# Kernel optimization log

Measured on AMD Instinct MI355X. Metric: run time of the kernel, lower is better.

Reference implementation:

```python
import jax, jax.numpy as jnp
import numpy as np

B, T, D_IN, D_OUT, N_HEAD = 2, 2048, 1024, 1024, 16
HEAD_DIM = D_OUT // N_HEAD


def setup_inputs() -> dict:
    key = jax.random.key(0)
    k1, k2, k3, k4 = jax.random.split(key, 4)
    s = 0.02  # init scale for weights
    return {
        "x": jax.random.normal(k1, (B, T, D_IN), jnp.float32),
        "Wq": jax.random.normal(k2, (D_OUT, D_IN), jnp.float32) * s,
        "Wk": jax.random.normal(k3, (D_OUT, D_IN), jnp.float32) * s,
        "Wv": jax.random.normal(k4, (D_OUT, D_IN), jnp.float32) * s,
    }


def reference(x, Wq, Wk, Wv):
    b, t, _ = x.shape
    h, hd = N_HEAD, HEAD_DIM
    # Linear projections (torch Linear: x @ W.T), split heads -> [b,h,t,hd]
    q = (x @ Wq.T).reshape(b, t, h, hd).transpose(0, 2, 1, 3)
    k = (x @ Wk.T).reshape(b, t, h, hd).transpose(0, 2, 1, 3)
    v = (x @ Wv.T).reshape(b, t, h, hd).transpose(0, 2, 1, 3)
    # raw scores [b,h,t,t], causal mask BEFORE scaling (as in source)
    omega = jnp.einsum("bhqd,bhkd->bhqk", q, k)
    causal = jnp.triu(jnp.ones((t, t), dtype=bool), k=1)
    omega = jnp.where(causal, -jnp.inf, omega)
    attw = jax.nn.softmax(omega / jnp.sqrt(jnp.asarray(hd, omega.dtype)), axis=-1)
    ctx = jnp.einsum("bhqk,bhkd->bhqd", attw, v)  # [b,h,t,hd]
    # Faithful to source: transpose(2,3) then view(B,T,d_out)
    out = jnp.swapaxes(ctx, 2, 3).reshape(b, t, D_OUT)
    return out
```

## Files before the change

kernel.cpp:

```cpp
#include <hip/hip_runtime.h>
#include <hip/hip_bf16.h>
#include <stdint.h>

typedef __attribute__((ext_vector_type(8))) short s16x8;
typedef __attribute__((ext_vector_type(4))) float f32x4;

#define T_   2048
#define NH   16
#define HD   64
#define DIN  1024
#define SCALE_LOG2 0.18033688011112042f

#define MFMA32(a, b, c) __builtin_amdgcn_mfma_f32_16x16x32_bf16(a, b, c, 0, 0, 0)

__device__ __forceinline__ unsigned short f2bf(float f) {
  union { float f; uint32_t u; } c; c.f = f;
  uint32_t u = c.u;
  return (unsigned short)((u + 0x7FFFu + ((u >> 16) & 1u)) >> 16);
}

__device__ __forceinline__ uint32_t pk_bf16(float a, float b) {
  __hip_bfloat162 h = __float22bfloat162_rn(make_float2(a, b));
  return *reinterpret_cast<uint32_t*>(&h);
}

#define GLL(gp, lp) __builtin_amdgcn_global_load_lds( \
    (__attribute__((address_space(1))) void*)(gp),    \
    (__attribute__((address_space(3))) void*)(lp), 16, 0, 0)

__global__ __launch_bounds__(256) void cvt_kernel(
    const float* __restrict__ x,  const float* __restrict__ wq,
    const float* __restrict__ wk, const float* __restrict__ wv,
    unsigned short* __restrict__ xb, unsigned short* __restrict__ wb) {
  int i = (blockIdx.x * 256 + threadIdx.x) * 4;
  float4 v;
  unsigned short* dp;
  if (i < 4194304) {
    v = *(const float4*)(x + i);
    dp = xb + i;
  } else {
    int j = i - 4194304;
    int seg = j >> 20, r = j & 1048575;
    const float* w = (seg == 0) ? wq : (seg == 1) ? wk : wv;
    v = *(const float4*)(w + r);
    dp = wb + j;
  }
  ushort4 o;
  o.x = f2bf(v.x); o.y = f2bf(v.y); o.z = f2bf(v.z); o.w = f2bf(v.w);
  *(ushort4*)dp = o;
}

__global__ __launch_bounds__(256) void qkv_gemm(
    const unsigned short* __restrict__ A, const unsigned short* __restrict__ Bm,
    unsigned short* __restrict__ qkv) {
  __shared__ __attribute__((aligned(16))) unsigned short Alds[64 * 64];
  __shared__ __attribute__((aligned(16))) unsigned short Blds[128 * 64];
  const int tid = threadIdx.x;
  const int lane = tid & 63, wave = tid >> 6;
  const int wm = wave >> 1, wn = wave & 1;
  const int m0 = blockIdx.y * 64, n0 = blockIdx.x * 128;

  f32x4 acc[2][4] = {};

  const int srA = wave * 16 + (lane >> 3);
  const int srB = wave * 32 + (lane >> 3);
  const int scol = (((lane & 7) ^ ((lane >> 3) & 7))) * 8;
  const unsigned short* ag = A  + (size_t)(m0 + srA) * DIN + scol;
  const unsigned short* bg = Bm + (size_t)(n0 + srB) * DIN + scol;
  unsigned short* al = &Alds[wave * 16 * 64];
  unsigned short* bl = &Blds[wave * 32 * 64];

  const int l16 = lane & 15, quad = lane >> 4;
  const int sw = l16 & 7;

  for (int k0 = 0; k0 < DIN; k0 += 64) {
    __syncthreads();
#pragma unroll
    for (int i = 0; i < 2; i++)
      GLL(ag + (size_t)i * 8 * DIN + k0, al + i * 512);
#pragma unroll
    for (int i = 0; i < 4; i++)
      GLL(bg + (size_t)i * 8 * DIN + k0, bl + i * 512);
    __syncthreads();
#pragma unroll
    for (int ks = 0; ks < 2; ks++) {
      const int cl = ((ks * 4 + quad) ^ sw) * 8;
      s16x8 af[2], bf[4];
#pragma unroll
      for (int mt = 0; mt < 2; mt++)
        af[mt] = *(const s16x8*)&Alds[(wm * 32 + mt * 16 + l16) * 64 + cl];
#pragma unroll
      for (int nt = 0; nt < 4; nt++)
        bf[nt] = *(const s16x8*)&Blds[(wn * 64 + nt * 16 + l16) * 64 + cl];
#pragma unroll
      for (int mt = 0; mt < 2; mt++)
#pragma unroll
        for (int nt = 0; nt < 4; nt++)
          acc[mt][nt] = MFMA32(af[mt], bf[nt], acc[mt][nt]);
    }
  }

#pragma unroll
  for (int mt = 0; mt < 2; mt++) {
    int mbase = m0 + wm * 32 + mt * 16 + (quad << 2);
    int b = mbase >> 11, t = mbase & 2047;
#pragma unroll
    for (int nt = 0; nt < 4; nt++) {
      int n = n0 + wn * 64 + nt * 16 + l16;
      int sel = n >> 10, h = (n >> 6) & 15, d = n & 63;
      int bh = b * NH + h;
      if (sel == 2) {
        ushort4 pk;
        pk.x = f2bf(acc[mt][nt][0]); pk.y = f2bf(acc[mt][nt][1]);
        pk.z = f2bf(acc[mt][nt][2]); pk.w = f2bf(acc[mt][nt][3]);
        *(ushort4*)&qkv[8388608 + (size_t)(bh * HD + d) * T_ + t] = pk;
      } else {
        float qs = (sel == 0) ? SCALE_LOG2 : 1.f;
#pragma unroll
        for (int r = 0; r < 4; r++)
          qkv[(size_t)sel * 4194304 + (size_t)(bh * T_ + t + r) * HD + d] =
              f2bf(acc[mt][nt][r] * qs);
      }
    }
  }
}

__global__ __launch_bounds__(256) void attn_kernel(
    const unsigned short* __restrict__ qkv, float* __restrict__ out) {
  __shared__ __attribute__((aligned(16))) unsigned short Klds[64 * 64];
  __shared__ __attribute__((aligned(16))) unsigned short Vt[64 * 64];
  __shared__ __attribute__((aligned(16))) unsigned short Plds[64 * 64];

  const int lane = threadIdx.x & 63, wave = threadIdx.x >> 6;
  const int l16 = lane & 15, quad = lane >> 4;
  const int swl = l16 & 7;
  const int qt = 31 - blockIdx.y, bh = blockIdx.x;
  const int q0 = qt * 64;
  const size_t bh_off = (size_t)bh * (T_ * HD);
  const unsigned short* Q  = qkv + bh_off;
  const unsigned short* Kb = qkv + 4194304 + bh_off;
  const unsigned short* Vb = qkv + 8388608 + bh_off;

  s16x8 qf[2];
  {
    const unsigned short* qp =
        Q + (size_t)(q0 + wave * 16 + l16) * HD + quad * 8;
    qf[0] = *(const s16x8*)(qp);
    qf[1] = *(const s16x8*)(qp + 32);
  }

  const int sr = threadIdx.x >> 3;
  const int sc = (threadIdx.x & 7) * 8;
  const int swc = (((threadIdx.x & 7) ^ (sr & 7))) * 8;

  s16x8 kr0 = *(const s16x8*)&Kb[(size_t)sr * HD + sc];
  s16x8 kr1 = *(const s16x8*)&Kb[(size_t)(sr + 32) * HD + sc];
  s16x8 vr0 = *(const s16x8*)&Vb[(size_t)sr * T_ + sc];
  s16x8 vr1 = *(const s16x8*)&Vb[(size_t)(sr + 32) * T_ + sc];

  const s16x8 onesf = {0x3F80, 0x3F80, 0x3F80, 0x3F80,
                       0x3F80, 0x3F80, 0x3F80, 0x3F80};
  f32x4 o[4] = {};
  f32x4 lacc = {};

  uint32_t* prow = (uint32_t*)&Plds[(wave * 16 + l16) * 64];
  const unsigned short* prd = &Plds[(wave * 16 + l16) * 64];

  for (int kt = 0; kt <= qt; kt++) {
    __syncthreads();
    *(s16x8*)&Klds[sr * 64 + swc] = kr0;
    *(s16x8*)&Klds[(sr + 32) * 64 + swc] = kr1;
    *(s16x8*)&Vt[sr * 64 + swc] = vr0;
    *(s16x8*)&Vt[(sr + 32) * 64 + swc] = vr1;
    if (kt < qt) {
      const unsigned short* kp = Kb + (size_t)(kt + 1) * 64 * HD;
      const unsigned short* vp = Vb + (kt + 1) * 64;
      kr0 = *(const s16x8*)&kp[(size_t)sr * HD + sc];
      kr1 = *(const s16x8*)&kp[(size_t)(sr + 32) * HD + sc];
      vr0 = *(const s16x8*)&vp[(size_t)sr * T_ + sc];
      vr1 = *(const s16x8*)&vp[(size_t)(sr + 32) * T_ + sc];
    }
    __syncthreads();

    f32x4 s[4] = {};
#pragma unroll
    for (int kk = 0; kk < 2; kk++) {
      const int cl = ((kk * 4 + quad) ^ swl) * 8;
#pragma unroll
      for (int nt = 0; nt < 4; nt++) {
        s16x8 kf = *(const s16x8*)&Klds[(nt * 16 + l16) * 64 + cl];
        s[nt] = MFMA32(kf, qf[kk], s[nt]);
      }
    }

    if (kt < qt) {
#pragma unroll
      for (int nt = 0; nt < 4; nt++) {
        float p0 = exp2f(s[nt][0]);
        float p1 = exp2f(s[nt][1]);
        float p2 = exp2f(s[nt][2]);
        float p3 = exp2f(s[nt][3]);
        *(uint2*)&prow[(((2 * nt + (quad >> 1)) ^ swl) << 2) + (quad & 1) * 2] =
            make_uint2(pk_bf16(p0, p1), pk_bf16(p2, p3));
      }
    } else {
      const int lim = wave * 16 + l16;
#pragma unroll
      for (int nt = 0; nt < 4; nt++) {
        const int kb = nt * 16 + quad * 4;
        float p0 = (kb + 0 <= lim) ? exp2f(s[nt][0]) : 0.f;
        float p1 = (kb + 1 <= lim) ? exp2f(s[nt][1]) : 0.f;
        float p2 = (kb + 2 <= lim) ? exp2f(s[nt][2]) : 0.f;
        float p3 = (kb + 3 <= lim) ? exp2f(s[nt][3]) : 0.f;
        *(uint2*)&prow[(((2 * nt + (quad >> 1)) ^ swl) << 2) + (quad & 1) * 2] =
            make_uint2(pk_bf16(p0, p1), pk_bf16(p2, p3));
      }
    }

#pragma unroll
    for (int kk = 0; kk < 2; kk++) {
      const int cl = ((kk * 4 + quad) ^ swl) * 8;
      s16x8 pf = *(const s16x8*)&prd[cl];
      lacc = MFMA32(pf, onesf, lacc);
#pragma unroll
      for (int dt = 0; dt < 4; dt++) {
        s16x8 vf = *(const s16x8*)&Vt[(dt * 16 + l16) * 64 + cl];
        o[dt] = MFMA32(pf, vf, o[dt]);
      }
    }
  }

  f32x4 inv;
#pragma unroll
  for (int r = 0; r < 4; r++) inv[r] = 1.f / lacc[r];
#pragma unroll
  for (int dt = 0; dt < 4; dt++) {
    float4 v = make_float4(o[dt][0] * inv[0], o[dt][1] * inv[1],
                           o[dt][2] * inv[2], o[dt][3] * inv[3]);
    *(float4*)(out + (size_t)bh * (HD * T_) + (size_t)(dt * 16 + l16) * T_ +
               q0 + wave * 16 + quad * 4) = v;
  }
}

extern "C" void kernel_launch(void* const* d_in, const int* in_sizes, int n_in,
                              void* d_out, int out_size, void* d_ws, size_t ws_size,
                              hipStream_t stream) {
  const float* x  = (const float*)d_in[0];
  const float* wq = (const float*)d_in[1];
  const float* wk = (const float*)d_in[2];
  const float* wv = (const float*)d_in[3];
  float* out = (float*)d_out;

  unsigned short* xb  = (unsigned short*)d_ws;
  unsigned short* wb  = xb + 4194304;
  unsigned short* qkv = wb + 3145728;

  cvt_kernel<<<7168, 256, 0, stream>>>(x, wq, wk, wv, xb, wb);
  dim3 g1(24, 64);
  qkv_gemm<<<g1, 256, 0, stream>>>(xb, wb, qkv);
  dim3 g2(32, 32);
  attn_kernel<<<g2, 256, 0, stream>>>(qkv, out);
}
```

Before: 150.5 us.

## Keep softmax probabilities in registers and feed PV via 16x16x16 MFMA

```diff
diff --git a/kernel.cpp b/kernel.cpp
--- a/kernel.cpp
+++ b/kernel.cpp
@@ -3,6 +3,7 @@
 #include <stdint.h>
 
 typedef __attribute__((ext_vector_type(8))) short s16x8;
+typedef __attribute__((ext_vector_type(4))) short s16x4;
 typedef __attribute__((ext_vector_type(4))) float f32x4;
 
 #define T_   2048
@@ -12,6 +13,16 @@
 #define SCALE_LOG2 0.18033688011112042f
 
 #define MFMA32(a, b, c) __builtin_amdgcn_mfma_f32_16x16x32_bf16(a, b, c, 0, 0, 0)
+
+__device__ __forceinline__ f32x4 mfma16(s16x4 a, s16x4 b, f32x4 c) {
+#if __has_builtin(__builtin_amdgcn_mfma_f32_16x16x16bf16_1k)
+  return __builtin_amdgcn_mfma_f32_16x16x16bf16_1k(a, b, c, 0, 0, 0);
+#else
+  s16x8 a8 = {a[0], a[1], a[2], a[3], 0, 0, 0, 0};
+  s16x8 b8 = {b[0], b[1], b[2], b[3], 0, 0, 0, 0};
+  return __builtin_amdgcn_mfma_f32_16x16x32_bf16(a8, b8, c, 0, 0, 0);
+#endif
+}
 
 __device__ __forceinline__ unsigned short f2bf(float f) {
   union { float f; uint32_t u; } c; c.f = f;
@@ -129,7 +140,6 @@
     const unsigned short* __restrict__ qkv, float* __restrict__ out) {
   __shared__ __attribute__((aligned(16))) unsigned short Klds[64 * 64];
   __shared__ __attribute__((aligned(16))) unsigned short Vt[64 * 64];
-  __shared__ __attribute__((aligned(16))) unsigned short Plds[64 * 64];
 
   const int lane = threadIdx.x & 63, wave = threadIdx.x >> 6;
   const int l16 = lane & 15, quad = lane >> 4;
@@ -158,13 +168,9 @@
   s16x8 vr0 = *(const s16x8*)&Vb[(size_t)sr * T_ + sc];
   s16x8 vr1 = *(const s16x8*)&Vb[(size_t)(sr + 32) * T_ + sc];
 
-  const s16x8 onesf = {0x3F80, 0x3F80, 0x3F80, 0x3F80,
-                       0x3F80, 0x3F80, 0x3F80, 0x3F80};
+  const s16x4 ones4 = {0x3F80, 0x3F80, 0x3F80, 0x3F80};
   f32x4 o[4] = {};
   f32x4 lacc = {};
-
-  uint32_t* prow = (uint32_t*)&Plds[(wave * 16 + l16) * 64];
-  const unsigned short* prd = &Plds[(wave * 16 + l16) * 64];
 
   for (int kt = 0; kt <= qt; kt++) {
     __syncthreads();
@@ -193,6 +199,7 @@
       }
     }
 
+    s16x4 pf[4];
     if (kt < qt) {
 #pragma unroll
       for (int nt = 0; nt < 4; nt++) {
@@ -200,8 +207,9 @@
         float p1 = exp2f(s[nt][1]);
         float p2 = exp2f(s[nt][2]);
         float p3 = exp2f(s[nt][3]);
-        *(uint2*)&prow[(((2 * nt + (quad >> 1)) ^ swl) << 2) + (quad & 1) * 2] =
-            make_uint2(pk_bf16(p0, p1), pk_bf16(p2, p3));
+        union { s16x4 v; uint2 u; } pu;
+        pu.u = make_uint2(pk_bf16(p0, p1), pk_bf16(p2, p3));
+        pf[nt] = pu.v;
       }
     } else {
       const int lim = wave * 16 + l16;
@@ -212,20 +220,23 @@
         float p1 = (kb + 1 <= lim) ? exp2f(s[nt][1]) : 0.f;
         float p2 = (kb + 2 <= lim) ? exp2f(s[nt][2]) : 0.f;
         float p3 = (kb + 3 <= lim) ? exp2f(s[nt][3]) : 0.f;
-        *(uint2*)&prow[(((2 * nt + (quad >> 1)) ^ swl) << 2) + (quad & 1) * 2] =
-            make_uint2(pk_bf16(p0, p1), pk_bf16(p2, p3));
-      }
-    }
-
-#pragma unroll
-    for (int kk = 0; kk < 2; kk++) {
-      const int cl = ((kk * 4 + quad) ^ swl) * 8;
-      s16x8 pf = *(const s16x8*)&prd[cl];
-      lacc = MFMA32(pf, onesf, lacc);
-#pragma unroll
-      for (int dt = 0; dt < 4; dt++) {
-        s16x8 vf = *(const s16x8*)&Vt[(dt * 16 + l16) * 64 + cl];
-        o[dt] = MFMA32(pf, vf, o[dt]);
+        union { s16x4 v; uint2 u; } pu;
+        pu.u = make_uint2(pk_bf16(p0, p1), pk_bf16(p2, p3));
+        pf[nt] = pu.v;
+      }
+    }
+
+#pragma unroll
+    for (int nt = 0; nt < 4; nt++)
+      lacc = mfma16(pf[nt], ones4, lacc);
+#pragma unroll
+    for (int dt = 0; dt < 4; dt++) {
+#pragma unroll
+      for (int nt = 0; nt < 4; nt++) {
+        s16x4 vf = *(const s16x4*)&Vt[(dt * 16 + l16) * 64 +
+                                      (((2 * nt + (quad >> 1)) ^ swl) << 3) +
+                                      (quad & 1) * 4];
+        o[dt] = mfma16(pf[nt], vf, o[dt]);
       }
     }
   }
```

New measurement: 154.0 us. 1.02x slower.
